# Optimization experiments

Hardware: AMD Instinct MI355X
Metric: run time of the kernel (lower is better)

## Reference

```python
import jax, jax.numpy as jnp
import numpy as np

B = 16384      # games
BS = 19        # board size
N2 = BS * BS   # 361
G = 8          # groups per board
S = 4          # stones per group
R = B * G      # total groups
K = R * S      # total stones
M = N2         # hash history length (H*W*history_factor)
I32MIN = np.iinfo(np.int32).min
I32MAX = np.iinfo(np.int32).max
NEG = jnp.float32(-1e9)


def setup_inputs() -> dict:
    key = jax.random.key(0)
    ks = jax.random.split(key, 10)
    logits = jax.random.normal(ks[0], (B, BS, BS), dtype=jnp.float32)
    legal_mask = jax.random.uniform(ks[1], (B, BS, BS)) < 0.7
    current_player = jax.random.randint(ks[2], (B,), 0, 2, dtype=jnp.int32)
    current_hash = jax.random.randint(ks[3], (B,), 0, I32MAX, dtype=jnp.int32)
    hash_history = jax.random.randint(ks[4], (B, M), 0, I32MAX, dtype=jnp.int32)
    move_count = jax.random.randint(ks[5], (B,), 0, M, dtype=jnp.int32)
    ZposT = jax.random.randint(ks[6], (3, N2), 0, I32MAX, dtype=jnp.int32)
    stone_global_index = jax.random.randint(ks[7], (K,), 0, N2, dtype=jnp.int32)
    stone_global_pointer = jnp.arange(R + 1, dtype=jnp.int32) * S          # CSR: stones per group
    group_global_pointer_per_board = jnp.arange(B + 1, dtype=jnp.int32) * G  # CSR: groups per board
    cap_idx = jax.random.randint(ks[8], (B, N2, 4), 0, G, dtype=jnp.int32)
    cap_on = jax.random.uniform(ks[9], (B, N2, 4)) < 0.05
    captured_group_local_index = jnp.where(cap_on, cap_idx, jnp.int32(-1))
    return {
        "logits": logits,
        "legal_mask": legal_mask,
        "current_player": current_player,
        "current_hash": current_hash,
        "hash_history": hash_history,
        "move_count": move_count,
        "ZposT": ZposT,
        "stone_global_index": stone_global_index,
        "stone_global_pointer": stone_global_pointer,
        "group_global_pointer_per_board": group_global_pointer_per_board,
        "captured_group_local_index": captured_group_local_index,
    }


def reference(logits, legal_mask, current_player, current_hash, hash_history,
              move_count, ZposT, stone_global_index, stone_global_pointer,
              group_global_pointer_per_board, captured_group_local_index):
    Bn, H, W = legal_mask.shape
    Rn = stone_global_pointer.shape[0] - 1
    Kn = stone_global_index.shape[0]
    z_empty, z_black, z_white = ZposT[0], ZposT[1], ZposT[2]

    # Placement delta: empty -> current player's stone, for every candidate point. (B, N2)
    placement_delta = z_empty[None, :] ^ jnp.where(
        (current_player == 0)[:, None], z_black[None, :], z_white[None, :])

    # Map each group -> board, each stone -> group (CSR expansion).
    groups_per_board = group_global_pointer_per_board[1:] - group_global_pointer_per_board[:-1]
    group_board = jnp.repeat(jnp.arange(Bn, dtype=jnp.int32), groups_per_board,
                             total_repeat_length=Rn)
    stones_per_group = stone_global_pointer[1:] - stone_global_pointer[:-1]
    group_for_stone = jnp.repeat(jnp.arange(Rn, dtype=jnp.int32), stones_per_group,
                                 total_repeat_length=Kn)
    stone_board = group_board[group_for_stone]

    # Per-stone removal delta: opponent stone -> empty.
    opp_for_stone = (1 - current_player)[stone_board]           # (K,)
    si = stone_global_index.astype(jnp.int32)
    z_opp = ZposT[1 + opp_for_stone, si]
    per_stone_delta = z_opp ^ z_empty[si]                        # (K,) int32

    # Segmented XOR reduction over each group's stones via XOR prefix scan.
    prefix = jax.lax.associative_scan(jnp.bitwise_xor, per_stone_delta)
    start = stone_global_pointer[:-1]
    end = stone_global_pointer[1:]
    end_val = prefix[jnp.clip(end - 1, 0)]
    start_val = jnp.where(start > 0, prefix[jnp.clip(start - 1, 0)], jnp.int32(0))
    group_xor = end_val ^ start_val                              # (R,) per-group removal delta

    # Gather capture deltas for up to 4 captured neighbor groups per candidate move.
    offs = group_global_pointer_per_board[:-1][:, None, None]    # (B,1,1)
    flat_ids = jnp.clip(captured_group_local_index, 0) + offs    # (B,N2,4)
    cap_vals = jnp.where(captured_group_local_index >= 0, group_xor[flat_ids], jnp.int32(0))
    capture_delta = cap_vals[..., 0] ^ cap_vals[..., 1] ^ cap_vals[..., 2] ^ cap_vals[..., 3]

    candidate = current_hash[:, None] ^ placement_delta ^ capture_delta  # (B, N2)

    # Super-ko repeat detection against hash history (mask, sort, searchsorted).
    Mh = hash_history.shape[1]
    valid = jnp.arange(Mh, dtype=jnp.int32)[None, :] < jnp.minimum(move_count, Mh)[:, None]
    masked_hist = jnp.where(valid, hash_history, jnp.int32(I32MIN))
    sorted_hist = jnp.sort(masked_hist, axis=1)
    idx = jnp.clip(
        jax.vmap(lambda h, c: jnp.searchsorted(h, c, side='right'))(sorted_hist, candidate) - 1,
        0)
    found = jnp.take_along_axis(sorted_hist, idx, axis=1)
    repeat = (found == candidate).reshape(Bn, H, W)

    final_mask = legal_mask & ~repeat
    return jnp.where(final_mask, logits, NEG)
```

## Files before the change

kernel.cpp:

```cpp
#include <hip/hip_runtime.h>
#include <stdint.h>

#define N2 361
#define BMW 1024u
#define EMPTY 0x80000000u
#define NEGV -998244352.0f

__global__ __launch_bounds__(256) void k_groups(
    const int* __restrict__ current_player,
    const int* __restrict__ ZposT,
    const int* __restrict__ stone_global_index,
    const int* __restrict__ stone_global_pointer,
    unsigned*  __restrict__ gx_out,
    const void* __restrict__ legal_raw,
    unsigned*  __restrict__ fmt_out,
    int packed_bits, int Rn)
{
    const int r = blockIdx.x * 256 + threadIdx.x;

    if (blockIdx.x == 0 && threadIdx.x < 64) {
        const int lane = threadIdx.x;
        const unsigned* lwd = (const unsigned*)legal_raw;
        const unsigned dv0 = lwd[lane];
        const unsigned dv1 = (lane < 27) ? lwd[64 + lane] : 0u;
        auto classify = [](unsigned v) -> unsigned {
            unsigned f = 0;
            #pragma unroll
            for (int j = 0; j < 4; ++j) {
                const unsigned bv = (v >> (8 * j)) & 0xFFu;
                if (bv > 1u) f |= 1u;
                if (j != 0 && bv != 0u) f |= 2u;
            }
            const unsigned x = v & 0xFFFFu, y = v >> 16;
            if ((x && x != 0x3F80u) || (y && y != 0x3F80u)) f |= 4u;
            if (x == 0x3F80u) f |= 8u;
            return f;
        };
        unsigned fcl = classify(dv0);
        if (lane < 27) fcl |= classify(dv1);
        unsigned fa = 0;
        fa |= __ballot(fcl & 1u) ? 1u : 0u;
        fa |= __ballot(fcl & 2u) ? 2u : 0u;
        fa |= __ballot(fcl & 4u) ? 4u : 0u;
        fa |= __ballot(fcl & 8u) ? 8u : 0u;
        unsigned fmt;
        if (packed_bits) fmt = 4u;
        else if (!(fa & 1u)) fmt = (fa & 2u) ? 1u : 0u;
        else if (!(fa & 4u)) fmt = (fa & 8u) ? 2u : 0u;
        else fmt = 1u;
        if (lane == 0) fmt_out[0] = fmt;
    }

    if (r < Rn) {
        const int sp0 = stone_global_pointer[r];
        const int sp1 = stone_global_pointer[r + 1];
        const int b   = r >> 3;
        const int cp  = current_player[b];
        const int opprow = (2 - cp) * N2;
        unsigned x = 0u;
        for (int k = sp0; k < sp1; ++k) {
            const int si = stone_global_index[k];
            x ^= (unsigned)ZposT[opprow + si] ^ (unsigned)ZposT[si];
        }
        gx_out[r] = x;
    }
}

__device__ __forceinline__ unsigned sel8(uint4 a, uint4 b, unsigned i) {
    const unsigned r01 = (i & 1u) ? a.y : a.x;
    const unsigned r23 = (i & 1u) ? a.w : a.z;
    const unsigned r45 = (i & 1u) ? b.y : b.x;
    const unsigned r67 = (i & 1u) ? b.w : b.z;
    const unsigned r03 = (i & 2u) ? r23 : r01;
    const unsigned r47 = (i & 2u) ? r67 : r45;
    return (i & 4u) ? r47 : r03;
}

__global__ __launch_bounds__(512) void k_main(
    const float* __restrict__ logits,
    const void*  __restrict__ legal_raw,
    const int*   __restrict__ current_hash,
    const int*   __restrict__ current_player,
    const int*   __restrict__ hash_history,
    const int*   __restrict__ move_count,
    const int*   __restrict__ ZposT,
    const int4*  __restrict__ captured4,
    const unsigned* __restrict__ gx_ws,
    const unsigned* __restrict__ fmt_ws,
    float* __restrict__ out)
{
    __shared__ unsigned s_bm[8 * BMW];
    const int tid  = threadIdx.x;
    const int wid  = tid >> 6;
    const int lane = tid & 63;
    const int b    = __builtin_amdgcn_readfirstlane(blockIdx.x * 8 + wid);
    unsigned* bm   = s_bm + wid * BMW;
    const size_t bbase = (size_t)b * N2;

    int cnt = move_count[b];
    cnt = cnt < 0 ? 0 : (cnt > N2 ? N2 : cnt);
    const int      fmt = (int)fmt_ws[0];
    const unsigned ch  = (unsigned)current_hash[b];
    const int      cp  = current_player[b];
    const uint4    ga  = *(const uint4*)(gx_ws + b * 8);
    const uint4    gb  = *(const uint4*)(gx_ws + b * 8 + 4);
    const int      prow = (1 + cp) * N2;

    const int*  hist  = hash_history + bbase;
    const int4* hist4 = (const int4*)hist;
    const int4  ha    = hist4[lane];
    const int4  hb    = (lane < 26) ? hist4[64 + lane] : int4{0,0,0,0};
    const int   hc    = (lane == 26) ? hist[360] : 0;

    int4 cap[6]; float lg[6]; unsigned zz[6]; unsigned leg[6];
    #pragma unroll
    for (int s = 0; s < 6; ++s) {
        const int n  = lane + 64 * s;
        const int nc = (n < N2) ? n : (N2 - 1);
        const size_t q = bbase + nc;
        cap[s] = captured4[q];
        lg[s]  = logits[q];
        zz[s]  = (unsigned)ZposT[nc] ^ (unsigned)ZposT[prow + nc];
        if (fmt == 0)      leg[s] = ((const unsigned*)legal_raw)[q];
        else if (fmt == 1) leg[s] = ((const uint8_t*)legal_raw)[q];
        else if (fmt == 2) leg[s] = ((const uint16_t*)legal_raw)[q];
        else               leg[s] = (((const uint8_t*)legal_raw)[q >> 3] >> (q & 7)) & 1u;
    }

    asm volatile("" ::: "memory");

    {
        uint4* t4 = (uint4*)bm;
        const uint4 z4 = {0u, 0u, 0u, 0u};
        #pragma unroll
        for (int i = 0; i < 4; ++i) t4[lane + 64 * i] = z4;
    }

    const int i0 = 4 * lane, i1 = 256 + 4 * lane;
    const unsigned e0 = (i0 + 0 < cnt) ? (unsigned)ha.x : EMPTY;
    const unsigned e1 = (i0 + 1 < cnt) ? (unsigned)ha.y : EMPTY;
    const unsigned e2 = (i0 + 2 < cnt) ? (unsigned)ha.z : EMPTY;
    const unsigned e3 = (i0 + 3 < cnt) ? (unsigned)ha.w : EMPTY;
    const unsigned e4 = (lane < 26 && i1 + 0 < cnt) ? (unsigned)hb.x : EMPTY;
    const unsigned e5 = (lane < 26 && i1 + 1 < cnt) ? (unsigned)hb.y : EMPTY;
    const unsigned e6 = (lane < 26 && i1 + 2 < cnt) ? (unsigned)hb.z : EMPTY;
    const unsigned e7 = (lane < 26 && i1 + 3 < cnt) ? (unsigned)hb.w : EMPTY;
    const unsigned e8 = (lane == 26 && 360 < cnt)   ? (unsigned)hc   : EMPTY;

    asm volatile("s_waitcnt lgkmcnt(0)" ::: "memory");
    __builtin_amdgcn_sched_barrier(0);

    auto setbit = [&](unsigned v) {
        if (!(v & EMPTY)) atomicOr(&bm[(v >> 5) & (BMW - 1u)], 1u << (v & 31u));
    };
    setbit(e0); setbit(e1); setbit(e2); setbit(e3);
    setbit(e4); setbit(e5); setbit(e6); setbit(e7); setbit(e8);

    unsigned cand[6];
    #pragma unroll
    for (int s = 0; s < 6; ++s) {
        unsigned capd = 0u;
        const int4 c = cap[s];
        if (c.x >= 0) capd ^= sel8(ga, gb, (unsigned)c.x & 7u);
        if (c.y >= 0) capd ^= sel8(ga, gb, (unsigned)c.y & 7u);
        if (c.z >= 0) capd ^= sel8(ga, gb, (unsigned)c.z & 7u);
        if (c.w >= 0) capd ^= sel8(ga, gb, (unsigned)c.w & 7u);
        cand[s] = ch ^ zz[s] ^ capd;
    }

    asm volatile("s_waitcnt lgkmcnt(0)" ::: "memory");
    __builtin_amdgcn_sched_barrier(0);

    unsigned bw[6];
    #pragma unroll
    for (int s = 0; s < 6; ++s) bw[s] = bm[(cand[s] >> 5) & (BMW - 1u)];

    auto match9 = [&](unsigned c) -> bool {
        return (e0 == c) | (e1 == c) | (e2 == c) | (e3 == c) |
               (e4 == c) | (e5 == c) | (e6 == c) | (e7 == c) | (e8 == c);
    };

    #pragma unroll
    for (int s = 0; s < 6; ++s) {
        const int n = lane + 64 * s;
        const bool inr = n < N2;
        bool rep = false;
        unsigned long long mask = __ballot(inr && ((bw[s] >> (cand[s] & 31u)) & 1u));
        while (mask) {
            const int l = __ffsll((unsigned long long)mask) - 1;
            const unsigned c = (unsigned)__shfl((int)cand[s], l);
            const unsigned long long fm = __ballot(match9(c));
            if (lane == l) rep = (fm != 0ull);
            mask &= mask - 1;
        }
        if (inr) {
            const float v = (leg[s] && !rep) ? lg[s] : NEGV;
            __builtin_nontemporal_store(v, &out[bbase + n]);
        }
    }
}

extern "C" void kernel_launch(void* const* d_in, const int* in_sizes, int n_in,
                              void* d_out, int out_size, void* d_ws, size_t ws_size,
                              hipStream_t stream) {
    const float* logits  = (const float*)d_in[0];
    const void*  legal   = (const void*)d_in[1];
    const int*   cur_pl  = (const int*)d_in[2];
    const int*   cur_h   = (const int*)d_in[3];
    const int*   hist    = (const int*)d_in[4];
    const int*   mcount  = (const int*)d_in[5];
    const int*   zpos    = (const int*)d_in[6];
    const int*   sgi     = (const int*)d_in[7];
    const int*   sgp     = (const int*)d_in[8];
    const int4*  cap4    = (const int4*)d_in[10];
    float*       out     = (float*)d_out;

    const int B  = in_sizes[2];
    const int Rn = in_sizes[8] - 1;
    const int packed = (in_sizes[1] != in_sizes[0]);

    unsigned* gx_ws  = (unsigned*)d_ws;
    unsigned* fmt_ws = (unsigned*)((char*)d_ws + (size_t)Rn * 4);

    k_groups<<<(Rn + 255) / 256, 256, 0, stream>>>(
        cur_pl, zpos, sgi, sgp, gx_ws, legal, fmt_ws, packed, Rn);

    k_main<<<B / 8, 512, 0, stream>>>(
        logits, legal, cur_h, cur_pl, hist, mcount, zpos,
        cap4, gx_ws, fmt_ws, out);
}
```

Measured before the change: 223.9 us.

## Replace per-wave bitmap filter with per-block open-addressing hash table

```diff
diff --git a/kernel.cpp b/kernel.cpp
--- a/kernel.cpp
+++ b/kernel.cpp
@@ -2,7 +2,8 @@
 #include <stdint.h>
 
 #define N2 361
-#define BMW 1024u
+#define TBL 1024u
+#define TBL_MASK 1023u
 #define EMPTY 0x80000000u
 #define NEGV -998244352.0f
 
@@ -76,7 +77,7 @@
     return (i & 4u) ? r47 : r03;
 }
 
-__global__ __launch_bounds__(512) void k_main(
+__global__ __launch_bounds__(384) void k_board(
     const float* __restrict__ logits,
     const void*  __restrict__ legal_raw,
     const int*   __restrict__ current_hash,
@@ -89,114 +90,72 @@
     const unsigned* __restrict__ fmt_ws,
     float* __restrict__ out)
 {
-    __shared__ unsigned s_bm[8 * BMW];
-    const int tid  = threadIdx.x;
-    const int wid  = tid >> 6;
-    const int lane = tid & 63;
-    const int b    = __builtin_amdgcn_readfirstlane(blockIdx.x * 8 + wid);
-    unsigned* bm   = s_bm + wid * BMW;
+    __shared__ unsigned s_tbl[TBL];
+
+    const int b = blockIdx.x;
+    const int t = threadIdx.x;
     const size_t bbase = (size_t)b * N2;
+    const bool act = t < N2;
+    const int tc = act ? t : (N2 - 1);
+    const size_t q = bbase + tc;
 
     int cnt = move_count[b];
     cnt = cnt < 0 ? 0 : (cnt > N2 ? N2 : cnt);
-    const int      fmt = (int)fmt_ws[0];
-    const unsigned ch  = (unsigned)current_hash[b];
-    const int      cp  = current_player[b];
-    const uint4    ga  = *(const uint4*)(gx_ws + b * 8);
-    const uint4    gb  = *(const uint4*)(gx_ws + b * 8 + 4);
+    const int      fmt  = (int)fmt_ws[0];
+    const unsigned ch   = (unsigned)current_hash[b];
+    const int      cp   = current_player[b];
+    const uint4    ga   = *(const uint4*)(gx_ws + b * 8);
+    const uint4    gb   = *(const uint4*)(gx_ws + b * 8 + 4);
     const int      prow = (1 + cp) * N2;
 
-    const int*  hist  = hash_history + bbase;
-    const int4* hist4 = (const int4*)hist;
-    const int4  ha    = hist4[lane];
-    const int4  hb    = (lane < 26) ? hist4[64 + lane] : int4{0,0,0,0};
-    const int   hc    = (lane == 26) ? hist[360] : 0;
+    const int   hv  = hash_history[q];
+    const int4  cap = captured4[q];
+    const float lgt = logits[q];
+    unsigned    leg;
+    if (fmt == 0)      leg = ((const unsigned*)legal_raw)[q];
+    else if (fmt == 1) leg = ((const uint8_t*)legal_raw)[q];
+    else if (fmt == 2) leg = ((const uint16_t*)legal_raw)[q];
+    else               leg = (((const uint8_t*)legal_raw)[q >> 3] >> (q & 7)) & 1u;
+    const unsigned zz = (unsigned)ZposT[tc] ^ (unsigned)ZposT[prow + tc];
 
-    int4 cap[6]; float lg[6]; unsigned zz[6]; unsigned leg[6];
-    #pragma unroll
-    for (int s = 0; s < 6; ++s) {
-        const int n  = lane + 64 * s;
-        const int nc = (n < N2) ? n : (N2 - 1);
-        const size_t q = bbase + nc;
-        cap[s] = captured4[q];
-        lg[s]  = logits[q];
-        zz[s]  = (unsigned)ZposT[nc] ^ (unsigned)ZposT[prow + nc];
-        if (fmt == 0)      leg[s] = ((const unsigned*)legal_raw)[q];
-        else if (fmt == 1) leg[s] = ((const uint8_t*)legal_raw)[q];
-        else if (fmt == 2) leg[s] = ((const uint16_t*)legal_raw)[q];
-        else               leg[s] = (((const uint8_t*)legal_raw)[q >> 3] >> (q & 7)) & 1u;
+    s_tbl[t] = EMPTY;
+    s_tbl[t + 384] = EMPTY;
+    if (t < (int)TBL - 768) s_tbl[t + 768] = EMPTY;
+    __syncthreads();
+
+    if (t < cnt) {
+        const unsigned v = (unsigned)hv;
+        unsigned slot = v & TBL_MASK;
+        while (true) {
+            const unsigned old = atomicCAS(&s_tbl[slot], EMPTY, v);
+            if (old == EMPTY || old == v) break;
+            slot = (slot + 1) & TBL_MASK;
+        }
     }
 
-    asm volatile("" ::: "memory");
+    unsigned capd = 0u;
+    if (cap.x >= 0) capd ^= sel8(ga, gb, (unsigned)cap.x & 7u);
+    if (cap.y >= 0) capd ^= sel8(ga, gb, (unsigned)cap.y & 7u);
+    if (cap.z >= 0) capd ^= sel8(ga, gb, (unsigned)cap.z & 7u);
+    if (cap.w >= 0) capd ^= sel8(ga, gb, (unsigned)cap.w & 7u);
+    const unsigned cand = ch ^ zz ^ capd;
 
+    __syncthreads();
+
+    bool rep = false;
     {
-        uint4* t4 = (uint4*)bm;
-        const uint4 z4 = {0u, 0u, 0u, 0u};
-        #pragma unroll
-        for (int i = 0; i < 4; ++i) t4[lane + 64 * i] = z4;
+        unsigned slot = cand & TBL_MASK;
+        while (true) {
+            const unsigned v = s_tbl[slot];
+            if (v == cand) { rep = true; break; }
+            if (v == EMPTY) break;
+            slot = (slot + 1) & TBL_MASK;
+        }
     }
 
-    const int i0 = 4 * lane, i1 = 256 + 4 * lane;
-    const unsigned e0 = (i0 + 0 < cnt) ? (unsigned)ha.x : EMPTY;
-    const unsigned e1 = (i0 + 1 < cnt) ? (unsigned)ha.y : EMPTY;
-    const unsigned e2 = (i0 + 2 < cnt) ? (unsigned)ha.z : EMPTY;
-    const unsigned e3 = (i0 + 3 < cnt) ? (unsigned)ha.w : EMPTY;
-    const unsigned e4 = (lane < 26 && i1 + 0 < cnt) ? (unsigned)hb.x : EMPTY;
-    const unsigned e5 = (lane < 26 && i1 + 1 < cnt) ? (unsigned)hb.y : EMPTY;
-    const unsigned e6 = (lane < 26 && i1 + 2 < cnt) ? (unsigned)hb.z : EMPTY;
-    const unsigned e7 = (lane < 26 && i1 + 3 < cnt) ? (unsigned)hb.w : EMPTY;
-    const unsigned e8 = (lane == 26 && 360 < cnt)   ? (unsigned)hc   : EMPTY;
-
-    asm volatile("s_waitcnt lgkmcnt(0)" ::: "memory");
-    __builtin_amdgcn_sched_barrier(0);
-
-    auto setbit = [&](unsigned v) {
-        if (!(v & EMPTY)) atomicOr(&bm[(v >> 5) & (BMW - 1u)], 1u << (v & 31u));
-    };
-    setbit(e0); setbit(e1); setbit(e2); setbit(e3);
-    setbit(e4); setbit(e5); setbit(e6); setbit(e7); setbit(e8);
-
-    unsigned cand[6];
-    #pragma unroll
-    for (int s = 0; s < 6; ++s) {
-        unsigned capd = 0u;
-        const int4 c = cap[s];
-        if (c.x >= 0) capd ^= sel8(ga, gb, (unsigned)c.x & 7u);
-        if (c.y >= 0) capd ^= sel8(ga, gb, (unsigned)c.y & 7u);
-        if (c.z >= 0) capd ^= sel8(ga, gb, (unsigned)c.z & 7u);
-        if (c.w >= 0) capd ^= sel8(ga, gb, (unsigned)c.w & 7u);
-        cand[s] = ch ^ zz[s] ^ capd;
-    }
-
-    asm volatile("s_waitcnt lgkmcnt(0)" ::: "memory");
-    __builtin_amdgcn_sched_barrier(0);
-
-    unsigned bw[6];
-    #pragma unroll
-    for (int s = 0; s < 6; ++s) bw[s] = bm[(cand[s] >> 5) & (BMW - 1u)];
-
-    auto match9 = [&](unsigned c) -> bool {
-        return (e0 == c) | (e1 == c) | (e2 == c) | (e3 == c) |
-               (e4 == c) | (e5 == c) | (e6 == c) | (e7 == c) | (e8 == c);
-    };
-
-    #pragma unroll
-    for (int s = 0; s < 6; ++s) {
-        const int n = lane + 64 * s;
-        const bool inr = n < N2;
-        bool rep = false;
-        unsigned long long mask = __ballot(inr && ((bw[s] >> (cand[s] & 31u)) & 1u));
-        while (mask) {
-            const int l = __ffsll((unsigned long long)mask) - 1;
-            const unsigned c = (unsigned)__shfl((int)cand[s], l);
-            const unsigned long long fm = __ballot(match9(c));
-            if (lane == l) rep = (fm != 0ull);
-            mask &= mask - 1;
-        }
-        if (inr) {
-            const float v = (leg[s] && !rep) ? lg[s] : NEGV;
-            __builtin_nontemporal_store(v, &out[bbase + n]);
-        }
+    if (act) {
+        const float v = (leg && !rep) ? lgt : NEGV;
+        __builtin_nontemporal_store(v, &out[q]);
     }
 }
 
@@ -225,7 +184,7 @@
     k_groups<<<(Rn + 255) / 256, 256, 0, stream>>>(
         cur_pl, zpos, sgi, sgp, gx_ws, legal, fmt_ws, packed, Rn);
 
-    k_main<<<B / 8, 512, 0, stream>>>(
+    k_board<<<B, 384, 0, stream>>>(
         logits, legal, cur_h, cur_pl, hist, mcount, zpos,
         cap4, gx_ws, fmt_ws, out);
 }
```

New measurement: 218.3 us. 1.03x faster.
